# Kernel tuning notes

Measured on AMD Instinct MI355X. Metric: run time of the kernel, lower is better.

Reference implementation:

```python
import jax, jax.numpy as jnp
import numpy as np
import itertools

D_FEAT = 8      # feature dim per point
N_NBR = 16     # kNN neighbors (self.N)
ORDERS = (2, 3)
BIG = 99999999.0


def _to_select(N, order):
    # rows: [0] + each (order-1)-combination of {1..N-1}, first N-1 rows
    rows = [[0] + list(c) for c in itertools.combinations(range(1, N), order - 1)][:N - 1]
    return np.asarray(rows, dtype=np.int32)  # (N-1, order)


def setup_inputs() -> dict:
    key = jax.random.key(0)
    ks = jax.random.split(key, 18)
    B, NP, DM, DO, NM, PNM = 4, 4096, 16, 8, 64, 64
    r = lambda k, s: jax.random.normal(k, s, dtype=jnp.float32)
    return {
        "x": r(ks[0], (B, NP * D_FEAT)),
        "z": r(ks[1], (B, PNM)),
        "Wm2": r(ks[2], (2, DM)) * 0.5, "bm2": r(ks[3], (DM,)) * 0.1,
        "Wm3": r(ks[4], (3, DM)) * 0.5, "bm3": r(ks[5], (DM,)) * 0.1,
        "Wv2": r(ks[6], (2, DM)) * 0.5, "bv2": r(ks[7], (DM,)) * 0.1,
        "Wv3": r(ks[8], (3, DM)) * 0.5, "bv3": r(ks[9], (DM,)) * 0.1,
        "Wmx": r(ks[10], (2 * DM, DO)) * 0.1, "bmx": r(ks[11], (DO,)) * 0.1,
        "Wvx": r(ks[12], (2 * DM, NM)) * 0.1, "bvx": r(ks[13], (NM,)) * 0.1,
        "Wmz": r(ks[14], (PNM, DO)) * 0.1, "bmz": r(ks[15], (DO,)) * 0.1,
        "Wvz": r(ks[16], (PNM, NM)) * 0.1, "bvz": r(ks[17], (NM,)) * 0.1,
    }


def _forward(x, z, Wm2, bm2, Wm3, bm3, Wv2, bv2, Wv3, bv3,
             Wmx, bmx, Wvx, bvx, Wmz, bmz, Wvz, bvz):
    B = x.shape[0]
    NP = x.shape[1] // D_FEAT
    N = N_NBR
    x3 = x.reshape(B, NP, D_FEAT)

    # pairwise euclidean distances via gram trick (avoids B*NP*NP*D intermediate)
    n2 = jnp.sum(x3 * x3, axis=-1)                                   # (B, NP)
    d2 = n2[:, :, None] + n2[:, None, :] - 2.0 * jnp.einsum('bid,bjd->bij', x3, x3)
    dist = jnp.sqrt(jnp.maximum(d2, 0.0))                            # (B, NP, NP)
    dist = jnp.where(dist == 0.0, BIG, dist)                         # mask exact-zero distances
    diag = jnp.arange(NP)
    dist = dist.at[:, diag, diag].set(BIG)                           # self-distance (exactly 0 in torch)

    # N smallest, sorted ascending
    _, idx = jax.lax.top_k(-dist, N)                                 # idx: (B, NP, N)

    def order_feats(Wf, bf, order):
        ts = jnp.asarray(_to_select(N, order))                       # (N-1, order)
        sel = idx[:, :, ts]                                          # (B, NP, N-1, o)
        g = jax.vmap(lambda xb, sb: xb[sb])(x3, sel)                 # (B, NP, N-1, o, D)
        # Linear(order -> d_Mfeat) applied per feature-dim o-tuple, relu, mean over feature dims
        y = jax.nn.relu(jnp.einsum('bnrod,ok->bnrdk', g, Wf) + bf)   # (B, NP, N-1, D, K)
        return y.mean(axis=3).reshape(B, NP * (N - 1), -1)           # (B, NP*(N-1), K)

    moments = jnp.concatenate([order_feats(Wm2, bm2, 2), order_feats(Wm3, bm3, 3)], axis=-1)
    v_moments = jnp.concatenate([order_feats(Wv2, bv2, 2), order_feats(Wv3, bv3, 3)], axis=-1)

    d_out = Wmx.shape[1]
    x_new = jax.nn.relu(moments @ Wmx + bmx + (z @ Wmz + bmz)[:, None, :])
    x_new = x_new.reshape(B, NP, N - 1, d_out).mean(axis=2).reshape(B, NP * d_out)

    z_new = jax.nn.relu(v_moments @ Wvx + bvx + (z @ Wvz + bvz)[:, None, :]).mean(axis=1)
    return x_new, z_new


def reference(x, z, Wm2, bm2, Wm3, bm3, Wv2, bv2, Wv3, bv3,
              Wmx, bmx, Wvx, bvx, Wmz, bmz, Wvz, bvz):
    return _forward(x, z, Wm2, bm2, Wm3, bm3, Wv2, bv2, Wv3, bv3,
                    Wmx, bmx, Wvx, bvx, Wmz, bmz, Wvz, bvz)
```

## Files before the change

kernel.cpp:

```cpp
#include <hip/hip_runtime.h>
#include <hip/hip_bf16.h>

#define BIGF 99999999.0f
#define NPP 4096
#define BB 4
#define NQ 2
#define CAP 128


template <typename T>
__device__ __forceinline__ T bitonic_sort64(T v, int lane) {
    #pragma unroll
    for (int k = 2; k <= 64; k <<= 1) {
        #pragma unroll
        for (int j = k >> 1; j > 0; j >>= 1) {
            T p = __shfl_xor(v, j);
            bool up  = ((lane & k) == 0);
            bool low = ((lane & j) == 0);
            T mn = (v < p) ? v : p;
            T mx = (v < p) ? p : v;
            v = (up == low) ? mn : mx;
        }
    }
    return v;
}


__global__ __launch_bounds__(256) void n2_kernel(
    const float* __restrict__ x, const float* __restrict__ z,
    const float* __restrict__ Wmz, const float* __restrict__ bmz,
    const float* __restrict__ Wvz, const float* __restrict__ bvz,
    float* __restrict__ n2tab, float* __restrict__ zzm, float* __restrict__ zzv,
    float* __restrict__ zout)
{
    int i = blockIdx.x * 256 + threadIdx.x;
    const float4* p = (const float4*)(x + (long)i * 8);
    float4 a = p[0], c = p[1];
    float s = 0.f;
    s = fmaf(a.x, a.x, s); s = fmaf(a.y, a.y, s);
    s = fmaf(a.z, a.z, s); s = fmaf(a.w, a.w, s);
    s = fmaf(c.x, c.x, s); s = fmaf(c.y, c.y, s);
    s = fmaf(c.z, c.z, s); s = fmaf(c.w, c.w, s);
    n2tab[i] = s;

    if (blockIdx.x == 0) {
        zout[threadIdx.x] = 0.f;
        int b = threadIdx.x >> 6, l = threadIdx.x & 63;
        float sv = 0.f;
        for (int q = 0; q < 64; ++q) sv = fmaf(z[b * 64 + q], Wvz[q * 64 + l], sv);
        zzv[b * 64 + l] = sv + bvz[l];
        if (threadIdx.x < 32) {
            int bm = threadIdx.x >> 3, lm = threadIdx.x & 7;
            float sm = 0.f;
            for (int q = 0; q < 64; ++q) sm = fmaf(z[bm * 64 + q], Wmz[q * 8 + lm], sm);
            zzm[bm * 8 + lm] = sm + bmz[lm];
        }
    }
}


__global__ __launch_bounds__(256) void knn_kernel(const float* __restrict__ x,
                                                  const float* __restrict__ n2tab,
                                                  int* __restrict__ idx_out) {
    __shared__ unsigned long long cand[4][NQ][CAP];
    __shared__ unsigned cnt_s[4][NQ];

    int lane = threadIdx.x & 63;
    int wid  = threadIdx.x >> 6;
    if (lane < NQ) cnt_s[wid][lane] = 0;

    int gw   = blockIdx.x * 4 + wid;
    int q0   = gw * NQ;
    int b    = q0 >> 12;
    int qloc = q0 & 4095;
    const float* xb = x + (long)b * NPP * 8;
    const float* nb = n2tab + b * NPP;

    float qf[NQ][8];
    float n2i[NQ];
    int selfT[NQ], selfL[NQ];
    #pragma unroll
    for (int q = 0; q < NQ; ++q) {
        #pragma unroll
        for (int f = 0; f < 8; ++f) qf[q][f] = xb[(qloc + q) * 8 + f];
        n2i[q]   = nb[qloc + q];
        selfT[q] = (qloc + q) >> 6;
        selfL[q] = (qloc + q) & 63;
    }
    const unsigned BIGB = __float_as_uint(BIGF);

    unsigned minb[NQ];
    #pragma unroll
    for (int q = 0; q < NQ; ++q) minb[q] = 0xFFFFFFFFu;

    #pragma unroll 4
    for (int t = 0; t < 64; ++t) {
        int j = t * 64 + lane;
        const float4* pj = (const float4*)(xb + (long)j * 8);
        float4 a = pj[0], c = pj[1];
        float n2j = nb[j];
        #pragma unroll
        for (int q = 0; q < NQ; ++q) {
            float dot = 0.f;
            dot = fmaf(qf[q][0], a.x, dot); dot = fmaf(qf[q][1], a.y, dot);
            dot = fmaf(qf[q][2], a.z, dot); dot = fmaf(qf[q][3], a.w, dot);
            dot = fmaf(qf[q][4], c.x, dot); dot = fmaf(qf[q][5], c.y, dot);
            dot = fmaf(qf[q][6], c.z, dot); dot = fmaf(qf[q][7], c.w, dot);
            float d2 = fmaf(-2.0f, dot, n2i[q] + n2j);
            unsigned kb = (d2 <= 0.0f) ? BIGB : __float_as_uint(d2);
            if (t == selfT[q]) {
                kb = (lane == selfL[q]) ? BIGB : kb;
            }
            minb[q] = (kb < minb[q]) ? kb : minb[q];
        }
    }

    unsigned T[NQ];
    #pragma unroll
    for (int q = 0; q < NQ; ++q) {
        unsigned s = bitonic_sort64(minb[q], lane);
        T[q] = (unsigned)__shfl((int)s, 15);
    }

    #pragma unroll 4
    for (int t = 0; t < 64; ++t) {
        int j = t * 64 + lane;
        const float4* pj = (const float4*)(xb + (long)j * 8);
        float4 a = pj[0], c = pj[1];
        float n2j = nb[j];
        unsigned kb[NQ];
        bool hit = false;
        #pragma unroll
        for (int q = 0; q < NQ; ++q) {
            float dot = 0.f;
            dot = fmaf(qf[q][0], a.x, dot); dot = fmaf(qf[q][1], a.y, dot);
            dot = fmaf(qf[q][2], a.z, dot); dot = fmaf(qf[q][3], a.w, dot);
            dot = fmaf(qf[q][4], c.x, dot); dot = fmaf(qf[q][5], c.y, dot);
            dot = fmaf(qf[q][6], c.z, dot); dot = fmaf(qf[q][7], c.w, dot);
            float d2 = fmaf(-2.0f, dot, n2i[q] + n2j);
            unsigned k = (d2 <= 0.0f) ? BIGB : __float_as_uint(d2);
            if (t == selfT[q]) {
                k = (lane == selfL[q]) ? BIGB : k;
            }
            kb[q] = k;
            hit |= (k <= T[q]);
        }
        if (__any(hit)) {
            #pragma unroll
            for (int q = 0; q < NQ; ++q) {
                if (kb[q] <= T[q]) {
                    unsigned old = atomicAdd(&cnt_s[wid][q], 1u);
                    if (old < CAP) {
                        cand[wid][q][old] =
                            ((unsigned long long)kb[q] << 32) | (unsigned)j;
                    }
                }
            }
        }
    }

    #pragma unroll 1
    for (int q = 0; q < NQ; ++q) {
        unsigned nc = cnt_s[wid][q];
        int n = nc > CAP ? CAP : (int)nc;
        unsigned long long v = (lane < n) ? cand[wid][q][lane] : ~0ull;
        unsigned long long R = bitonic_sort64(v, lane);
        if (n > 64) {
            unsigned long long w2 = (64 + lane < n) ? cand[wid][q][64 + lane] : ~0ull;
            w2 = bitonic_sort64(w2, lane);
            unsigned long long vt = __shfl(w2, lane - 16);
            unsigned long long comb = (lane < 16) ? R : ((lane < 32) ? vt : ~0ull);
            R = bitonic_sort64(comb, lane);
        }
        if (lane < 16) {
            idx_out[(long)(q0 + q) * 16 + lane] = (int)(R & 0xFFFFFFFFull);
        }
    }
}


__global__ __launch_bounds__(256) void feat_kernel(
    const float* __restrict__ x, const int* __restrict__ idxw,
    const float* __restrict__ Wm2, const float* __restrict__ bm2,
    const float* __restrict__ Wm3, const float* __restrict__ bm3,
    const float* __restrict__ Wv2, const float* __restrict__ bv2,
    const float* __restrict__ Wv3, const float* __restrict__ bv3,
    const float* __restrict__ Wmx, const float* __restrict__ bmx,
    const float* __restrict__ Wvx, const float* __restrict__ bvx,
    const float* __restrict__ zzm, const float* __restrict__ zzv,
    float* __restrict__ xout, float* __restrict__ zout)
{
    int lane = threadIdx.x & 63;
    int wid  = threadIdx.x >> 6;
    int pn   = blockIdx.x * 4 + wid;
    int b    = pn >> 12;
    const float* xb = x + b * NPP * 8;

    __shared__ float xg_s[4][16][8];
    __shared__ float mo_s[4][15][68];
    __shared__ float wmx_s[32][8];
    __shared__ float bzm_s[8];
    __shared__ float zpart[4][64];

    if (threadIdx.x < 256) {
        wmx_s[threadIdx.x >> 3][threadIdx.x & 7] = Wmx[threadIdx.x];
    }
    if (threadIdx.x < 8) bzm_s[threadIdx.x] = bmx[threadIdx.x] + zzm[b * 8 + threadIdx.x];

    int k = lane & 15;
    float w20 = Wm2[k], w21 = Wm2[16 + k], bb2 = bm2[k];
    float w30 = Wm3[k], w31 = Wm3[16 + k], w32 = Wm3[32 + k], bb3 = bm3[k];
    float u20 = Wv2[k], u21 = Wv2[16 + k], cc2 = bv2[k];
    float u30 = Wv3[k], u31 = Wv3[16 + k], u32 = Wv3[32 + k], cc3 = bv3[k];
    float wvx[32];
    #pragma unroll
    for (int c = 0; c < 32; ++c) wvx[c] = Wvx[c * 64 + lane];
    float bz3 = bvx[lane] + zzv[b * 64 + lane];

    if (lane < 16) {
        int myid = idxw[(long)pn * 16 + lane];
        const float4* ps = (const float4*)(xb + (long)myid * 8);
        float4 a = ps[0], c4 = ps[1];
        *((float4*)&xg_s[wid][lane][0]) = a;
        *((float4*)&xg_s[wid][lane][4]) = c4;
    }
    __syncthreads();

    float g0[8];
    #pragma unroll
    for (int f = 0; f < 8; ++f) g0[f] = xg_s[wid][0][f];

    #pragma unroll
    for (int p = 0; p < 4; ++p) {
        int rg = lane >> 4;
        int r  = p * 4 + rg;
        int rc = (r < 14) ? r : 14;
        int i2  = rc + 1;
        int i3a = (rc < 14) ? 1 : 2;
        int i3b = (rc < 14) ? rc + 2 : 3;
        const float* G1  = xg_s[wid][i2];
        const float* G3a = xg_s[wid][i3a];
        const float* G3b = xg_s[wid][i3b];
        float s2 = 0.f, s3 = 0.f, t2 = 0.f, t3 = 0.f;
        #pragma unroll
        for (int d = 0; d < 8; ++d) {
            float gz = g0[d], g1 = G1[d], ga = G3a[d], gb = G3b[d];
            float y2 = fmaf(gz, w20, fmaf(g1, w21, bb2));
            s2 += fmaxf(y2, 0.f);
            float y3 = fmaf(gz, w30, fmaf(ga, w31, fmaf(gb, w32, bb3)));
            s3 += fmaxf(y3, 0.f);
            float z2 = fmaf(gz, u20, fmaf(g1, u21, cc2));
            t2 += fmaxf(z2, 0.f);
            float z3 = fmaf(gz, u30, fmaf(ga, u31, fmaf(gb, u32, cc3)));
            t3 += fmaxf(z3, 0.f);
        }
        if (r < 15) {
            mo_s[wid][r][k]      = s2 * 0.125f;
            mo_s[wid][r][16 + k] = s3 * 0.125f;
            mo_s[wid][r][32 + k] = t2 * 0.125f;
            mo_s[wid][r][48 + k] = t3 * 0.125f;
        }
    }
    __syncthreads();

    float xa = 0.f;
    #pragma unroll
    for (int half = 0; half < 2; ++half) {
        int r   = (lane >> 3) + half * 8;
        int doo = lane & 7;
        float s = 0.f;
        if (r < 15) {
            s = bzm_s[doo];
            #pragma unroll
            for (int cc = 0; cc < 8; ++cc) {
                float4 v = *(const float4*)&mo_s[wid][r][cc * 4];
                s = fmaf(v.x, wmx_s[cc * 4 + 0][doo], s);
                s = fmaf(v.y, wmx_s[cc * 4 + 1][doo], s);
                s = fmaf(v.z, wmx_s[cc * 4 + 2][doo], s);
                s = fmaf(v.w, wmx_s[cc * 4 + 3][doo], s);
            }
            s = fmaxf(s, 0.f);
        }
        xa += s;
    }
    xa += __shfl_xor(xa, 8);
    xa += __shfl_xor(xa, 16);
    xa += __shfl_xor(xa, 32);
    float xv = xa * (1.0f / 15.0f);
    if (lane < 8) xout[(long)pn * 8 + lane] = xv;

    float za = 0.f;
    #pragma unroll 1
    for (int r = 0; r < 15; ++r) {
        const float* row = &mo_s[wid][r][32];
        float s = bz3;
        #pragma unroll
        for (int cc = 0; cc < 8; ++cc) {
            float4 v = *(const float4*)(row + cc * 4);
            s = fmaf(v.x, wvx[cc * 4 + 0], s);
            s = fmaf(v.y, wvx[cc * 4 + 1], s);
            s = fmaf(v.z, wvx[cc * 4 + 2], s);
            s = fmaf(v.w, wvx[cc * 4 + 3], s);
        }
        za += fmaxf(s, 0.f);
    }
    za *= (1.0f / 61440.0f);

    zpart[wid][lane] = za;
    __syncthreads();
    if (wid == 0) {
        float ssum = zpart[0][lane] + zpart[1][lane] + zpart[2][lane] + zpart[3][lane];
        atomicAdd(&zout[b * 64 + lane], ssum);
    }
}


extern "C" void kernel_launch(void* const* d_in, const int* in_sizes, int n_in,
                              void* d_out, int out_size, void* d_ws, size_t ws_size,
                              hipStream_t stream) {
    const float* x   = (const float*)d_in[0];
    const float* z   = (const float*)d_in[1];
    const float* Wm2 = (const float*)d_in[2];
    const float* bm2 = (const float*)d_in[3];
    const float* Wm3 = (const float*)d_in[4];
    const float* bm3 = (const float*)d_in[5];
    const float* Wv2 = (const float*)d_in[6];
    const float* bv2 = (const float*)d_in[7];
    const float* Wv3 = (const float*)d_in[8];
    const float* bv3 = (const float*)d_in[9];
    const float* Wmx = (const float*)d_in[10];
    const float* bmx = (const float*)d_in[11];
    const float* Wvx = (const float*)d_in[12];
    const float* bvx = (const float*)d_in[13];
    const float* Wmz = (const float*)d_in[14];
    const float* bmz = (const float*)d_in[15];
    const float* Wvz = (const float*)d_in[16];
    const float* bvz = (const float*)d_in[17];

    float* out  = (float*)d_out;
    int*   idxw = (int*)d_ws;
    float* zzm  = (float*)((char*)d_ws + (size_t)BB * NPP * 16 * 4);
    float* zzv  = zzm + BB * 8;
    float* n2t  = zzv + BB * 64;
    float* xout = out;
    float* zout = out + BB * NPP * 8;

    n2_kernel<<<dim3(BB * NPP / 256), dim3(256), 0, stream>>>(
        x, z, Wmz, bmz, Wvz, bvz, n2t, zzm, zzv, zout);
    knn_kernel<<<dim3(BB * NPP / (4 * NQ)), dim3(256), 0, stream>>>(x, n2t, idxw);
    feat_kernel<<<dim3(4096), dim3(256), 0, stream>>>(
        x, idxw, Wm2, bm2, Wm3, bm3, Wv2, bv2, Wv3, bv3,
        Wmx, bmx, Wvx, bvx, zzm, zzv, xout, zout);
}
```

Before: 245.8 us.

## Process four queries per wave with packed FMA and restructure feature-stage loops

The kNN kernel now handles four queries per wavefront instead of two, so each loaded candidate point is reused across more queries. Its dot products use v_pk_fma_f32 on float pairs. In the feature kernel, Wmx is stored transposed in shared memory for float4 reads, the gather rows are read as float4, and the Wvx projection splits rows between the two half-waves with a shuffle reduction. The risks are higher register pressure from four queries plus 64 Wvx registers, half as many kNN blocks, and candidate-buffer contention with four query slots per wave.

```diff
diff --git a/kernel.cpp b/kernel.cpp
--- a/kernel.cpp
+++ b/kernel.cpp
@@ -4,8 +4,16 @@
 #define BIGF 99999999.0f
 #define NPP 4096
 #define BB 4
-#define NQ 2
+#define NQ 4
 #define CAP 128
+
+typedef float f32x2 __attribute__((ext_vector_type(2)));
+
+__device__ __forceinline__ f32x2 pk_fma(f32x2 a, f32x2 b, f32x2 c) {
+    f32x2 d;
+    asm("v_pk_fma_f32 %0, %1, %2, %3" : "=v"(d) : "v"(a), "v"(b), "v"(c));
+    return d;
+}
 
 
 template <typename T>
@@ -23,6 +31,16 @@
         }
     }
     return v;
+}
+
+__device__ __forceinline__ float dot8_pk(const f32x2* qp, f32x2 p0, f32x2 p1,
+                                         f32x2 p2, f32x2 p3) {
+    f32x2 acc = {0.f, 0.f};
+    acc = pk_fma(qp[0], p0, acc);
+    acc = pk_fma(qp[1], p1, acc);
+    acc = pk_fma(qp[2], p2, acc);
+    acc = pk_fma(qp[3], p3, acc);
+    return acc.x + acc.y;
 }
 
 
@@ -76,13 +94,14 @@
     const float* xb = x + (long)b * NPP * 8;
     const float* nb = n2tab + b * NPP;
 
-    float qf[NQ][8];
+    f32x2 qp[NQ][4];
     float n2i[NQ];
     int selfT[NQ], selfL[NQ];
     #pragma unroll
     for (int q = 0; q < NQ; ++q) {
-        #pragma unroll
-        for (int f = 0; f < 8; ++f) qf[q][f] = xb[(qloc + q) * 8 + f];
+        const f32x2* qsrc = (const f32x2*)(xb + (long)(qloc + q) * 8);
+        #pragma unroll
+        for (int e = 0; e < 4; ++e) qp[q][e] = qsrc[e];
         n2i[q]   = nb[qloc + q];
         selfT[q] = (qloc + q) >> 6;
         selfL[q] = (qloc + q) & 63;
@@ -96,17 +115,13 @@
     #pragma unroll 4
     for (int t = 0; t < 64; ++t) {
         int j = t * 64 + lane;
-        const float4* pj = (const float4*)(xb + (long)j * 8);
-        float4 a = pj[0], c = pj[1];
+        const f32x2* pj = (const f32x2*)(xb + (long)j * 8);
+        f32x2 p0 = pj[0], p1 = pj[1], p2 = pj[2], p3 = pj[3];
         float n2j = nb[j];
         #pragma unroll
         for (int q = 0; q < NQ; ++q) {
-            float dot = 0.f;
-            dot = fmaf(qf[q][0], a.x, dot); dot = fmaf(qf[q][1], a.y, dot);
-            dot = fmaf(qf[q][2], a.z, dot); dot = fmaf(qf[q][3], a.w, dot);
-            dot = fmaf(qf[q][4], c.x, dot); dot = fmaf(qf[q][5], c.y, dot);
-            dot = fmaf(qf[q][6], c.z, dot); dot = fmaf(qf[q][7], c.w, dot);
-            float d2 = fmaf(-2.0f, dot, n2i[q] + n2j);
+            float dot = dot8_pk(qp[q], p0, p1, p2, p3);
+            float d2  = fmaf(-2.0f, dot, n2i[q] + n2j);
             unsigned kb = (d2 <= 0.0f) ? BIGB : __float_as_uint(d2);
             if (t == selfT[q]) {
                 kb = (lane == selfL[q]) ? BIGB : kb;
@@ -125,19 +140,15 @@
     #pragma unroll 4
     for (int t = 0; t < 64; ++t) {
         int j = t * 64 + lane;
-        const float4* pj = (const float4*)(xb + (long)j * 8);
-        float4 a = pj[0], c = pj[1];
+        const f32x2* pj = (const f32x2*)(xb + (long)j * 8);
+        f32x2 p0 = pj[0], p1 = pj[1], p2 = pj[2], p3 = pj[3];
         float n2j = nb[j];
         unsigned kb[NQ];
         bool hit = false;
         #pragma unroll
         for (int q = 0; q < NQ; ++q) {
-            float dot = 0.f;
-            dot = fmaf(qf[q][0], a.x, dot); dot = fmaf(qf[q][1], a.y, dot);
-            dot = fmaf(qf[q][2], a.z, dot); dot = fmaf(qf[q][3], a.w, dot);
-            dot = fmaf(qf[q][4], c.x, dot); dot = fmaf(qf[q][5], c.y, dot);
-            dot = fmaf(qf[q][6], c.z, dot); dot = fmaf(qf[q][7], c.w, dot);
-            float d2 = fmaf(-2.0f, dot, n2i[q] + n2j);
+            float dot = dot8_pk(qp[q], p0, p1, p2, p3);
+            float d2  = fmaf(-2.0f, dot, n2i[q] + n2j);
             unsigned k = (d2 <= 0.0f) ? BIGB : __float_as_uint(d2);
             if (t == selfT[q]) {
                 k = (lane == selfL[q]) ? BIGB : k;
@@ -198,12 +209,12 @@
 
     __shared__ float xg_s[4][16][8];
     __shared__ float mo_s[4][15][68];
-    __shared__ float wmx_s[32][8];
+    __shared__ float wmxT_s[8][36];
     __shared__ float bzm_s[8];
     __shared__ float zpart[4][64];
 
     if (threadIdx.x < 256) {
-        wmx_s[threadIdx.x >> 3][threadIdx.x & 7] = Wmx[threadIdx.x];
+        wmxT_s[threadIdx.x & 7][threadIdx.x >> 3] = Wmx[threadIdx.x];
     }
     if (threadIdx.x < 8) bzm_s[threadIdx.x] = bmx[threadIdx.x] + zzm[b * 8 + threadIdx.x];
 
@@ -212,10 +223,17 @@
     float w30 = Wm3[k], w31 = Wm3[16 + k], w32 = Wm3[32 + k], bb3 = bm3[k];
     float u20 = Wv2[k], u21 = Wv2[16 + k], cc2 = bv2[k];
     float u30 = Wv3[k], u31 = Wv3[16 + k], u32 = Wv3[32 + k], cc3 = bv3[k];
-    float wvx[32];
-    #pragma unroll
-    for (int c = 0; c < 32; ++c) wvx[c] = Wvx[c * 64 + lane];
-    float bz3 = bvx[lane] + zzv[b * 64 + lane];
+
+    int g  = lane >> 5;
+    int nm = lane & 31;
+    float wvxa[32], wvxb[32];
+    #pragma unroll
+    for (int c = 0; c < 32; ++c) {
+        wvxa[c] = Wvx[c * 64 + nm];
+        wvxb[c] = Wvx[c * 64 + nm + 32];
+    }
+    float bz3a = bvx[nm]      + zzv[b * 64 + nm];
+    float bz3b = bvx[nm + 32] + zzv[b * 64 + nm + 32];
 
     if (lane < 16) {
         int myid = idxw[(long)pn * 16 + lane];
@@ -226,9 +244,9 @@
     }
     __syncthreads();
 
-    float g0[8];
-    #pragma unroll
-    for (int f = 0; f < 8; ++f) g0[f] = xg_s[wid][0][f];
+    float4 g0l = *(const float4*)&xg_s[wid][0][0];
+    float4 g0h = *(const float4*)&xg_s[wid][0][4];
+    float g0[8] = {g0l.x, g0l.y, g0l.z, g0l.w, g0h.x, g0h.y, g0h.z, g0h.w};
 
     #pragma unroll
     for (int p = 0; p < 4; ++p) {
@@ -238,9 +256,15 @@
         int i2  = rc + 1;
         int i3a = (rc < 14) ? 1 : 2;
         int i3b = (rc < 14) ? rc + 2 : 3;
-        const float* G1  = xg_s[wid][i2];
-        const float* G3a = xg_s[wid][i3a];
-        const float* G3b = xg_s[wid][i3b];
+        float4 a1 = *(const float4*)&xg_s[wid][i2][0];
+        float4 b1 = *(const float4*)&xg_s[wid][i2][4];
+        float4 aa = *(const float4*)&xg_s[wid][i3a][0];
+        float4 ba = *(const float4*)&xg_s[wid][i3a][4];
+        float4 ab = *(const float4*)&xg_s[wid][i3b][0];
+        float4 bb = *(const float4*)&xg_s[wid][i3b][4];
+        float G1[8]  = {a1.x, a1.y, a1.z, a1.w, b1.x, b1.y, b1.z, b1.w};
+        float G3a[8] = {aa.x, aa.y, aa.z, aa.w, ba.x, ba.y, ba.z, ba.w};
+        float G3b[8] = {ab.x, ab.y, ab.z, ab.w, bb.x, bb.y, bb.z, bb.w};
         float s2 = 0.f, s3 = 0.f, t2 = 0.f, t3 = 0.f;
         #pragma unroll
         for (int d = 0; d < 8; ++d) {
@@ -274,10 +298,11 @@
             #pragma unroll
             for (int cc = 0; cc < 8; ++cc) {
                 float4 v = *(const float4*)&mo_s[wid][r][cc * 4];
-                s = fmaf(v.x, wmx_s[cc * 4 + 0][doo], s);
-                s = fmaf(v.y, wmx_s[cc * 4 + 1][doo], s);
-                s = fmaf(v.z, wmx_s[cc * 4 + 2][doo], s);
-                s = fmaf(v.w, wmx_s[cc * 4 + 3][doo], s);
+                float4 w = *(const float4*)&wmxT_s[doo][cc * 4];
+                s = fmaf(v.x, w.x, s);
+                s = fmaf(v.y, w.y, s);
+                s = fmaf(v.z, w.z, s);
+                s = fmaf(v.w, w.w, s);
             }
             s = fmaxf(s, 0.f);
         }
@@ -289,23 +314,32 @@
     float xv = xa * (1.0f / 15.0f);
     if (lane < 8) xout[(long)pn * 8 + lane] = xv;
 
-    float za = 0.f;
+    float A = 0.f, Bz = 0.f;
     #pragma unroll 1
-    for (int r = 0; r < 15; ++r) {
-        const float* row = &mo_s[wid][r][32];
-        float s = bz3;
-        #pragma unroll
-        for (int cc = 0; cc < 8; ++cc) {
-            float4 v = *(const float4*)(row + cc * 4);
-            s = fmaf(v.x, wvx[cc * 4 + 0], s);
-            s = fmaf(v.y, wvx[cc * 4 + 1], s);
-            s = fmaf(v.z, wvx[cc * 4 + 2], s);
-            s = fmaf(v.w, wvx[cc * 4 + 3], s);
-        }
-        za += fmaxf(s, 0.f);
-    }
-    za *= (1.0f / 61440.0f);
-
+    for (int rr = 0; rr < 8; ++rr) {
+        int r = g * 8 + rr;
+        if (r < 15) {
+            const float* row = &mo_s[wid][r][32];
+            float sa = bz3a, sb = bz3b;
+            #pragma unroll
+            for (int cc = 0; cc < 8; ++cc) {
+                float4 v = *(const float4*)(row + cc * 4);
+                sa = fmaf(v.x, wvxa[cc * 4 + 0], sa);
+                sb = fmaf(v.x, wvxb[cc * 4 + 0], sb);
+                sa = fmaf(v.y, wvxa[cc * 4 + 1], sa);
+                sb = fmaf(v.y, wvxb[cc * 4 + 1], sb);
+                sa = fmaf(v.z, wvxa[cc * 4 + 2], sa);
+                sb = fmaf(v.z, wvxb[cc * 4 + 2], sb);
+                sa = fmaf(v.w, wvxa[cc * 4 + 3], sa);
+                sb = fmaf(v.w, wvxb[cc * 4 + 3], sb);
+            }
+            A  += fmaxf(sa, 0.f);
+            Bz += fmaxf(sb, 0.f);
+        }
+    }
+    A  += __shfl_xor(A, 32);
+    Bz += __shfl_xor(Bz, 32);
+    float za = ((g == 0) ? A : Bz) * (1.0f / 61440.0f);
     zpart[wid][lane] = za;
     __syncthreads();
     if (wid == 0) {
```

New measurement: 241.1 us. About the same (-1.9%).
